# Performance work log

Measured on AMD Instinct MI355X. Metric: run time of the kernel, lower is better.

## Reference

```python
import jax, jax.numpy as jnp
import numpy as np

B, S, D = 4, 4096, 256

def setup_inputs() -> dict:
    key = jax.random.key(0)
    ks = jax.random.split(key, 7)
    s = 1.0 / np.sqrt(D)
    return {
        "x": jax.random.normal(ks[0], (B, S, D), dtype=jnp.float32),
        "Wq": jax.random.uniform(ks[1], (D, D), jnp.float32, -s, s),
        "bq": jax.random.uniform(ks[2], (D,), jnp.float32, -s, s),
        "Wk": jax.random.uniform(ks[3], (D, D), jnp.float32, -s, s),
        "bk": jax.random.uniform(ks[4], (D,), jnp.float32, -s, s),
        "Wv": jax.random.uniform(ks[5], (D, D), jnp.float32, -s, s),
        "bv": jax.random.uniform(ks[6], (D,), jnp.float32, -s, s),
    }

def reference(x, Wq, bq, Wk, bk, Wv, bv):
    q = x @ Wq + bq            # [B,S,D]
    k = x @ Wk + bk
    v = x @ Wv + bv
    scores = jnp.einsum('bqd,bkd->bqk', q, k) / jnp.sqrt(jnp.float32(D))
    attn = jax.nn.softmax(scores, axis=-1)  # [B,S,S]
    return jnp.einsum('bqk,bkd->bqd', attn, v)
```

## Files before the change

kernel.cpp:

```cpp
#include <hip/hip_runtime.h>

typedef short v8s __attribute__((ext_vector_type(8)));
typedef float v4f __attribute__((ext_vector_type(4)));
typedef unsigned short u16;
typedef unsigned int u32;
typedef u16 v4u __attribute__((ext_vector_type(4)));

#define SS 4096
#define DD 256
#define QB 128
#define KVB 32

__device__ __forceinline__ u16 f2bf(float f) {
  u32 u = __builtin_bit_cast(u32, f);
  return (u16)((u + 0x7FFFu + ((u >> 16) & 1u)) >> 16);
}

__device__ __forceinline__ void gload16(const u16* g, u16* l) {
  __builtin_amdgcn_global_load_lds((const __attribute__((address_space(1))) u32*)g,
                                   (__attribute__((address_space(3))) u32*)l, 16, 0, 0);
}

__global__ void wcast_kernel(const float* __restrict__ Wq, const float* __restrict__ Wk,
                             const float* __restrict__ Wv, u16* __restrict__ wt) {
  int f = blockIdx.x * 256 + threadIdx.x;
  int p = f >> 16, rem = f & 65535, n = rem >> 8, k = rem & 255;
  const float* W = (p == 0) ? Wq : ((p == 1) ? Wk : Wv);
  wt[f] = f2bf(W[k * 256 + n]);
}

__global__ __launch_bounds__(256) void proj_kernel(
    const float* __restrict__ x, const u16* __restrict__ wt,
    const float* __restrict__ bq, const float* __restrict__ bk, const float* __restrict__ bv,
    u16* __restrict__ qg, u16* __restrict__ kg, u16* __restrict__ vtg) {
  __shared__ u16 xs[64 * 256];
  const int tid = threadIdx.x;
  const int lane = tid & 63, w = tid >> 6, g = lane >> 4, l15 = lane & 15;
  const int tok0 = blockIdx.x * 64;

#pragma unroll
  for (int it = 0; it < 8; ++it) {
    int idx = it * 256 + tid;
    int r = idx >> 5, d0 = (idx & 31) << 3;
    const float* src = x + (size_t)(tok0 + r) * DD + d0;
    float4 a = *(const float4*)src;
    float4 bb = *(const float4*)(src + 4);
    v8s pk;
    pk[0] = (short)f2bf(a.x);  pk[1] = (short)f2bf(a.y);
    pk[2] = (short)f2bf(a.z);  pk[3] = (short)f2bf(a.w);
    pk[4] = (short)f2bf(bb.x); pk[5] = (short)f2bf(bb.y);
    pk[6] = (short)f2bf(bb.z); pk[7] = (short)f2bf(bb.w);
    *(v8s*)(xs + r * DD + (((d0 >> 3) ^ (r & 7)) << 3)) = pk;
  }
  __syncthreads();

  v8s af[4][8];
#pragma unroll
  for (int m = 0; m < 4; ++m) {
    const int row = 16 * m + l15;
#pragma unroll
    for (int c = 0; c < 8; ++c)
      af[m][c] = *(const v8s*)(xs + row * DD + ((((4 * c + g) ^ (row & 7))) << 3));
  }

  const float SCL = 0.0625f * 1.44269504088896f;
  for (int p = 0; p < 3; ++p) {
    const u16* wbase = wt + p * 65536;
    const float* bias = (p == 0) ? bq : ((p == 1) ? bk : bv);
    v4f acc[4][4];
    const v4f vzero = {0.f, 0.f, 0.f, 0.f};
#pragma unroll
    for (int m = 0; m < 4; ++m)
#pragma unroll
      for (int t = 0; t < 4; ++t) acc[m][t] = vzero;
#pragma unroll
    for (int t = 0; t < 4; ++t) {
      const int n = 64 * w + 16 * t + l15;
      const u16* wrow = wbase + n * 256;
#pragma unroll
      for (int c = 0; c < 8; ++c) {
        v8s bf = *(const v8s*)(wrow + 8 * g + 32 * c);
#pragma unroll
        for (int m = 0; m < 4; ++m)
          acc[m][t] = __builtin_amdgcn_mfma_f32_16x16x32_bf16(af[m][c], bf, acc[m][t], 0, 0, 0);
      }
    }
    if (p == 0) {
#pragma unroll
      for (int t = 0; t < 4; ++t) {
        int n = 64 * w + 16 * t + l15;
        float bb = bias[n];
#pragma unroll
        for (int m = 0; m < 4; ++m)
#pragma unroll
          for (int r = 0; r < 4; ++r)
            qg[(size_t)(tok0 + 16 * m + 4 * g + r) * DD + n] = f2bf((acc[m][t][r] + bb) * SCL);
      }
    } else if (p == 1) {
#pragma unroll
      for (int t = 0; t < 4; ++t) {
        int n = 64 * w + 16 * t + l15;
        float bb = bias[n];
#pragma unroll
        for (int m = 0; m < 4; ++m)
#pragma unroll
          for (int r = 0; r < 4; ++r)
            kg[(size_t)(tok0 + 16 * m + 4 * g + r) * DD + n] = f2bf(acc[m][t][r] + bb);
      }
    } else {
      const int b = tok0 >> 12;
      const int s0 = tok0 & 4095;
#pragma unroll
      for (int t = 0; t < 4; ++t) {
        int n = 64 * w + 16 * t + l15;
        float bb = bias[n];
#pragma unroll
        for (int m = 0; m < 4; ++m) {
          v4u pk;
#pragma unroll
          for (int r = 0; r < 4; ++r) pk[r] = f2bf(acc[m][t][r] + bb);
          *(v4u*)(vtg + (size_t)(b * DD + n) * SS + s0 + 16 * m + 4 * g) = pk;
        }
      }
    }
  }
}

#define STAGE(kt_, buf_)                                                          \
  {                                                                               \
    const int kt__ = (kt_);                                                       \
    u16* kd = kb + (buf_)*8192;                                                   \
    u16* vd = vt + (buf_)*8192;                                                   \
    _Pragma("unroll")                                                             \
    for (int it = 0; it < 4; ++it) {                                              \
      int idx = it * 256 + tid;                                                   \
      int ch = idx >> 6, tt = ch >> 3, cc = ch & 7;                               \
      int ll = (idx >> 2) & 15, gp = (idx & 3) ^ (ll & 3);                        \
      gload16(kbase + (size_t)(kt__ * KVB + 16 * tt + ll) * DD + 8 * (4 * cc + gp), \
              kd + idx * 8);                                                      \
    }                                                                             \
    _Pragma("unroll")                                                             \
    for (int it = 0; it < 4; ++it) {                                              \
      int idx = it * 256 + tid;                                                   \
      int tt = idx >> 6, ll = (idx >> 2) & 15, gp = (idx & 3) ^ (ll & 3);         \
      gload16(vbase + (size_t)(16 * tt + ll) * SS + kt__ * KVB + 8 * gp,          \
              vd + idx * 8);                                                      \
    }                                                                             \
  }

__global__ __attribute__((amdgpu_flat_work_group_size(256, 256),
                          amdgpu_waves_per_eu(2))) void attn_kernel(
    const u16* __restrict__ qg, const u16* __restrict__ kg, const u16* __restrict__ vtg,
    float* __restrict__ o0, float* __restrict__ opart, float* __restrict__ ml,
    int nsplit, int nblk) {
  extern __shared__ u16 sm[];
  u16* kb = sm;
  u16* vt = sm + 16384;

  const int bid = blockIdx.x;
  const int lg = (bid & 7) * (nblk >> 3) + (bid >> 3);
  const int slice = lg >> 7;
  const int rem = lg & 127;
  const int b = rem >> 5;
  const int qt = rem & 31;
  const int NT = (SS / KVB) / nsplit;
  const int koff = slice * (SS / nsplit);

  const int tid = threadIdx.x;
  const int lane = tid & 63, w = tid >> 6, g = lane >> 4, l15 = lane & 15;
  const int slot = ((l15 << 2) | (g ^ (l15 & 3))) << 3;

  const u16* qbase = qg + (size_t)(b * SS + qt * QB) * DD;
  const u16* kbase = kg + (size_t)(b * SS + koff) * DD;
  const u16* vbase = vtg + (size_t)b * DD * SS + koff;

  STAGE(0, 0);

  v8s qf[2][8];
#pragma unroll
  for (int j = 0; j < 2; ++j) {
    const u16* qr = qbase + (size_t)(32 * w + 16 * j + l15) * DD;
#pragma unroll
    for (int c = 0; c < 8; ++c)
      qf[j][c] = *(const v8s*)(qr + ((4 * c + g) << 3));
  }

  float mrow[2], lrow[2];
  v4f oacc[2][16];
  const v4f vzero = {0.f, 0.f, 0.f, 0.f};
#pragma unroll
  for (int j = 0; j < 2; ++j) { mrow[j] = -1e30f; lrow[j] = 0.f; }
#pragma unroll
  for (int m = 0; m < 2; ++m)
#pragma unroll
    for (int t = 0; t < 16; ++t) oacc[m][t] = vzero;

  for (int kt = 0; kt < NT; ++kt) {
    const int cur = kt & 1;
    __syncthreads();
    if (kt + 1 < NT) STAGE(kt + 1, cur ^ 1);
    const u16* kc = kb + cur * 8192;
    const u16* vc = vt + cur * 8192;

    v4f sacc[2][2];
#pragma unroll
    for (int t = 0; t < 2; ++t)
#pragma unroll
      for (int j = 0; j < 2; ++j) sacc[t][j] = vzero;
    __builtin_amdgcn_s_setprio(1);
#pragma unroll
    for (int c = 0; c < 8; ++c) {
#pragma unroll
      for (int t = 0; t < 2; ++t) {
        v8s kf = *(const v8s*)(kc + (((t << 3) | c) << 9) + slot);
#pragma unroll
        for (int j = 0; j < 2; ++j)
          sacc[t][j] = __builtin_amdgcn_mfma_f32_16x16x32_bf16(kf, qf[j][c], sacc[t][j], 0, 0, 0);
      }
    }
    __builtin_amdgcn_s_setprio(0);

    float tml[2];
#pragma unroll
    for (int j = 0; j < 2; ++j) {
      float a0 = fmaxf(fmaxf(sacc[0][j][0], sacc[0][j][1]), fmaxf(sacc[0][j][2], sacc[0][j][3]));
      float a1 = fmaxf(fmaxf(sacc[1][j][0], sacc[1][j][1]), fmaxf(sacc[1][j][2], sacc[1][j][3]));
      tml[j] = fmaxf(a0, a1);
    }
    const bool ok = (tml[0] - mrow[0] <= 11.0f) && (tml[1] - mrow[1] <= 11.0f);
    if (!__all(ok)) {
      float sc[2];
#pragma unroll
      for (int j = 0; j < 2; ++j) {
        float t0 = fmaxf(tml[j], __shfl_xor(tml[j], 16));
        t0 = fmaxf(t0, __shfl_xor(t0, 32));
        float nm = fmaxf(mrow[j], t0);
        sc[j] = exp2f(mrow[j] - nm);
        mrow[j] = nm;
        lrow[j] *= sc[j];
      }
#pragma unroll
      for (int m = 0; m < 2; ++m) {
#pragma unroll
        for (int r = 0; r < 4; ++r) {
          float s4 = __shfl(sc[m], (lane & 48) | (4 * g + r));
#pragma unroll
          for (int t = 0; t < 16; ++t) oacc[m][t][r] *= s4;
        }
      }
    }

    v8s pa[2];
#pragma unroll
    for (int j = 0; j < 2; ++j) {
      u32 m32[4];
      float ls = 0.f;
#pragma unroll
      for (int t = 0; t < 2; ++t) {
        float e0 = exp2f(sacc[t][j][0] - mrow[j]);
        float e1 = exp2f(sacc[t][j][1] - mrow[j]);
        float e2 = exp2f(sacc[t][j][2] - mrow[j]);
        float e3 = exp2f(sacc[t][j][3] - mrow[j]);
        ls += (e0 + e1) + (e2 + e3);
        u32 lo, hi;
        asm("v_cvt_pk_bf16_f32 %0, %1, %2" : "=v"(lo) : "v"(e0), "v"(e1));
        asm("v_cvt_pk_bf16_f32 %0, %1, %2" : "=v"(hi) : "v"(e2), "v"(e3));
        m32[2 * t] = lo;
        m32[2 * t + 1] = hi;
      }
      lrow[j] += ls;
      const int la = l15 | ((g & 1) << 5);
      const int lb = la + 16;
      u32 A0 = (u32)__shfl((int)m32[0], la), A2 = (u32)__shfl((int)m32[2], la);
      u32 B1 = (u32)__shfl((int)m32[1], la), B3 = (u32)__shfl((int)m32[3], la);
      u32 C0 = (u32)__shfl((int)m32[0], lb), C2 = (u32)__shfl((int)m32[2], lb);
      u32 D1 = (u32)__shfl((int)m32[1], lb), D3 = (u32)__shfl((int)m32[3], lb);
      const bool sel = ((g >> 1) & 1) != 0;
      union { v8s v; u32 u[4]; } P;
      P.u[0] = sel ? A2 : A0;
      P.u[1] = sel ? B3 : B1;
      P.u[2] = sel ? C2 : C0;
      P.u[3] = sel ? D3 : D1;
      pa[j] = P.v;
    }

    __builtin_amdgcn_s_setprio(1);
#pragma unroll
    for (int t = 0; t < 16; ++t) {
      v8s bvv = *(const v8s*)(vc + (t << 9) + slot);
#pragma unroll
      for (int m = 0; m < 2; ++m)
        oacc[m][t] = __builtin_amdgcn_mfma_f32_16x16x32_bf16(pa[m], bvv, oacc[m][t], 0, 0, 0);
    }
    __builtin_amdgcn_s_setprio(0);
  }

#pragma unroll
  for (int j = 0; j < 2; ++j) {
    lrow[j] += __shfl_xor(lrow[j], 16);
    lrow[j] += __shfl_xor(lrow[j], 32);
  }
  float* ob = (slice == 0) ? o0 : (opart + (size_t)(slice - 1) * 4194304);
  const size_t rb = (size_t)b * SS + (size_t)qt * QB;
  if (g == 0) {
#pragma unroll
    for (int j = 0; j < 2; ++j) {
      const size_t rowg = rb + 32 * w + 16 * j + l15;
      float2 v2 = make_float2(mrow[j], lrow[j]);
      *(float2*)(ml + ((size_t)slice * 16384 + rowg) * 2) = v2;
    }
  }
#pragma unroll
  for (int m = 0; m < 2; ++m)
#pragma unroll
    for (int t = 0; t < 16; ++t)
#pragma unroll
      for (int r = 0; r < 4; ++r)
        ob[(rb + 32 * w + 16 * m + 4 * g + r) * DD + 16 * t + l15] = oacc[m][t][r];
}

__global__ __launch_bounds__(256) void combine_kernel(
    float* __restrict__ out, const float* __restrict__ opart,
    const float* __restrict__ ml, int nsplit) {
  const int tid = threadIdx.x;
  const size_t row = (size_t)blockIdx.x * 4 + (tid >> 6);
  const int d = (tid & 63) * 4;
  float2 mls[4];
  float mm = -1e30f;
#pragma unroll
  for (int s = 0; s < 4; ++s) {
    if (s < nsplit) {
      mls[s] = *(const float2*)(ml + ((size_t)s * 16384 + row) * 2);
      mm = fmaxf(mm, mls[s].x);
    }
  }
  float l = 0.f;
  float4 acc = {0.f, 0.f, 0.f, 0.f};
#pragma unroll
  for (int s = 0; s < 4; ++s) {
    if (s < nsplit) {
      float a = exp2f(mls[s].x - mm);
      const float* src = (s == 0) ? (out + row * DD + d)
                                  : (opart + (size_t)(s - 1) * 4194304 + row * DD + d);
      float4 v = *(const float4*)src;
      l += a * mls[s].y;
      acc.x += a * v.x; acc.y += a * v.y; acc.z += a * v.z; acc.w += a * v.w;
    }
  }
  float inv = 1.0f / l;
  acc.x *= inv; acc.y *= inv; acc.z *= inv; acc.w *= inv;
  *(float4*)(out + row * DD + d) = acc;
}

extern "C" void kernel_launch(void* const* d_in, const int* in_sizes, int n_in,
                              void* d_out, int out_size, void* d_ws, size_t ws_size,
                              hipStream_t stream) {
  const float* x  = (const float*)d_in[0];
  const float* Wq = (const float*)d_in[1];
  const float* bq = (const float*)d_in[2];
  const float* Wk = (const float*)d_in[3];
  const float* bk = (const float*)d_in[4];
  const float* Wv = (const float*)d_in[5];
  const float* bv = (const float*)d_in[6];
  float* out = (float*)d_out;
  char* ws = (char*)d_ws;

  u16* wt    = (u16*)ws;
  u16* qg    = (u16*)(ws + 393216);
  u16* kg    = (u16*)(ws + 393216 + 8388608);
  u16* vtg   = (u16*)(ws + 393216 + 2 * 8388608);
  float* ml  = (float*)(ws + 25559040);
  float* op  = (float*)(ws + 26083328);
  const size_t need4 = 26083328ull + 3ull * 16777216ull;
  const size_t need2 = 26083328ull + 1ull * 16777216ull;
  const int nsplit = (ws_size >= need4) ? 4 : ((ws_size >= need2) ? 2 : 1);
  const int nblk = 128 * nsplit;

  (void)hipFuncSetAttribute((const void*)attn_kernel,
                            hipFuncAttributeMaxDynamicSharedMemorySize, 65536);

  wcast_kernel<<<dim3(768), dim3(256), 0, stream>>>(Wq, Wk, Wv, wt);
  proj_kernel<<<dim3(256), dim3(256), 0, stream>>>(x, wt, bq, bk, bv, qg, kg, vtg);
  attn_kernel<<<dim3(nblk), dim3(256), 65536, stream>>>(qg, kg, vtg, out, op, ml, nsplit, nblk);
  combine_kernel<<<dim3(4096), dim3(256), 0, stream>>>(out, op, ml, nsplit);
}
```

Baseline: 148.5 us.

## Fuse split-KV combine into attention kernel via last-block atomic counter

Removes the separate combine kernel launch. Each attention block bumps a per-query-tile atomic counter after writing its partial output and softmax stats, and the last-arriving split block merges all partials for that tile. This drops one kernel launch and its tail, but adds a memset, threadfences and a serialized combine pass done by one block per tile.

```diff
diff --git a/kernel.cpp b/kernel.cpp
--- a/kernel.cpp
+++ b/kernel.cpp
@@ -152,7 +152,7 @@
                           amdgpu_waves_per_eu(2))) void attn_kernel(
     const u16* __restrict__ qg, const u16* __restrict__ kg, const u16* __restrict__ vtg,
     float* __restrict__ o0, float* __restrict__ opart, float* __restrict__ ml,
-    int nsplit, int nblk) {
+    int* __restrict__ cnt, int nsplit, int nblk) {
   extern __shared__ u16 sm[];
   u16* kb = sm;
   u16* vt = sm + 16384;
@@ -317,39 +317,45 @@
 #pragma unroll
       for (int r = 0; r < 4; ++r)
         ob[(rb + 32 * w + 16 * m + 4 * g + r) * DD + 16 * t + l15] = oacc[m][t][r];
-}
-
-__global__ __launch_bounds__(256) void combine_kernel(
-    float* __restrict__ out, const float* __restrict__ opart,
-    const float* __restrict__ ml, int nsplit) {
-  const int tid = threadIdx.x;
-  const size_t row = (size_t)blockIdx.x * 4 + (tid >> 6);
-  const int d = (tid & 63) * 4;
-  float2 mls[4];
-  float mm = -1e30f;
-#pragma unroll
-  for (int s = 0; s < 4; ++s) {
-    if (s < nsplit) {
-      mls[s] = *(const float2*)(ml + ((size_t)s * 16384 + row) * 2);
-      mm = fmaxf(mm, mls[s].x);
-    }
-  }
-  float l = 0.f;
-  float4 acc = {0.f, 0.f, 0.f, 0.f};
-#pragma unroll
-  for (int s = 0; s < 4; ++s) {
-    if (s < nsplit) {
-      float a = exp2f(mls[s].x - mm);
-      const float* src = (s == 0) ? (out + row * DD + d)
-                                  : (opart + (size_t)(s - 1) * 4194304 + row * DD + d);
-      float4 v = *(const float4*)src;
-      l += a * mls[s].y;
-      acc.x += a * v.x; acc.y += a * v.y; acc.z += a * v.z; acc.w += a * v.w;
-    }
-  }
-  float inv = 1.0f / l;
-  acc.x *= inv; acc.y *= inv; acc.z *= inv; acc.w *= inv;
-  *(float4*)(out + row * DD + d) = acc;
+
+  __syncthreads();
+  if (tid == 0) {
+    __threadfence();
+    ((int*)sm)[0] = atomicAdd(&cnt[rem], 1);
+  }
+  __syncthreads();
+  if (((int*)sm)[0] == nsplit - 1) {
+    __threadfence();
+    for (int i = tid; i < 128 * 64; i += 256) {
+      const int rl = i >> 6, d4 = (i & 63) << 2;
+      const size_t row = rb + rl;
+      float2 mls[4];
+      float mm = -1e30f;
+#pragma unroll
+      for (int s = 0; s < 4; ++s) {
+        if (s < nsplit) {
+          mls[s] = *(const float2*)(ml + ((size_t)s * 16384 + row) * 2);
+          mm = fmaxf(mm, mls[s].x);
+        }
+      }
+      float l = 0.f;
+      float4 acc = {0.f, 0.f, 0.f, 0.f};
+#pragma unroll
+      for (int s = 0; s < 4; ++s) {
+        if (s < nsplit) {
+          float a = exp2f(mls[s].x - mm);
+          const float* src = (s == 0) ? (o0 + row * DD + d4)
+                                      : (opart + (size_t)(s - 1) * 4194304 + row * DD + d4);
+          float4 v = *(const float4*)src;
+          l += a * mls[s].y;
+          acc.x += a * v.x; acc.y += a * v.y; acc.z += a * v.z; acc.w += a * v.w;
+        }
+      }
+      float inv = 1.0f / l;
+      acc.x *= inv; acc.y *= inv; acc.z *= inv; acc.w *= inv;
+      *(float4*)(o0 + row * DD + d4) = acc;
+    }
+  }
 }
 
 extern "C" void kernel_launch(void* const* d_in, const int* in_sizes, int n_in,
@@ -370,17 +376,19 @@
   u16* kg    = (u16*)(ws + 393216 + 8388608);
   u16* vtg   = (u16*)(ws + 393216 + 2 * 8388608);
   float* ml  = (float*)(ws + 25559040);
-  float* op  = (float*)(ws + 26083328);
-  const size_t need4 = 26083328ull + 3ull * 16777216ull;
-  const size_t need2 = 26083328ull + 1ull * 16777216ull;
+  int* cnt   = (int*)(ws + 26083328);
+  float* op  = (float*)(ws + 26083840);
+  const size_t need4 = 26083840ull + 3ull * 16777216ull;
+  const size_t need2 = 26083840ull + 1ull * 16777216ull;
   const int nsplit = (ws_size >= need4) ? 4 : ((ws_size >= need2) ? 2 : 1);
   const int nblk = 128 * nsplit;
 
   (void)hipFuncSetAttribute((const void*)attn_kernel,
                             hipFuncAttributeMaxDynamicSharedMemorySize, 65536);
 
+  (void)hipMemsetAsync(cnt, 0, 512, stream);
   wcast_kernel<<<dim3(768), dim3(256), 0, stream>>>(Wq, Wk, Wv, wt);
   proj_kernel<<<dim3(256), dim3(256), 0, stream>>>(x, wt, bq, bk, bv, qg, kg, vtg);
-  attn_kernel<<<dim3(nblk), dim3(256), 65536, stream>>>(qg, kg, vtg, out, op, ml, nsplit, nblk);
-  combine_kernel<<<dim3(4096), dim3(256), 0, stream>>>(out, op, ml, nsplit);
-}
+  attn_kernel<<<dim3(nblk), dim3(256), 65536, stream>>>(qg, kg, vtg, out, op, ml, cnt,
+                                                        nsplit, nblk);
+}
```

After: 259.1 us. 1.75x slower.
